# Performance work log

Hardware: AMD Instinct MI355X
Metric: run time of the kernel (lower is better)

The kernel has to match this reference:

```python
import jax, jax.numpy as jnp
import numpy as np

HID = 768
HEADS = 12
HEAD_LEN = HID // HEADS
SCALE_INV = 1.0 / np.sqrt(HEAD_LEN).astype(np.float32)


def setup_inputs() -> dict:
    key = jax.random.key(0)
    ks = jax.random.split(key, 5)
    std = 1.0 / np.sqrt(HID)
    return {
        "x": jax.random.normal(ks[0], (1, 4096, HID), dtype=jnp.float32),
        "w_q": jax.random.normal(ks[1], (HID, HID), dtype=jnp.float32) * std,
        "w_k": jax.random.normal(ks[2], (HID, HID), dtype=jnp.float32) * std,
        "w_v": jax.random.normal(ks[3], (HID, HID), dtype=jnp.float32) * std,
        "w_fc": jax.random.normal(ks[4], (HID, HID), dtype=jnp.float32) * std,
    }


def reference(x, w_q, w_k, w_v, w_fc):
    B, S, D = x.shape
    # torch Linear weight layout [out, in]: y = x @ W.T
    def proj_heads(w):
        y = jnp.einsum("bsd,ed->bse", x, w)
        return y.reshape(B, S, HEADS, HEAD_LEN).transpose(0, 2, 1, 3)  # bhsd
    q = proj_heads(w_q)
    k = proj_heads(w_k)
    v = proj_heads(w_v)
    scores = SCALE_INV * jnp.einsum("bhqd,bhkd->bhqk", q, k)
    attn = jax.nn.softmax(scores, axis=-1)
    out = jnp.einsum("bhqk,bhkd->bhqd", attn, v)
    out = out.transpose(0, 2, 1, 3).reshape(B, S, D)
    return jnp.einsum("bsd,ed->bse", out, w_fc)
```

## Files before the change

kernel.cpp:

```cpp
#include <hip/hip_runtime.h>
#include <hip/hip_bf16.h>

#define S_LEN 4096
#define HID 768
#define NHEAD 12
#define HL 64
#define QB 64
#define ORST 68

typedef __attribute__((ext_vector_type(8))) short short8;
typedef __attribute__((ext_vector_type(4))) short s16x4;
typedef __attribute__((ext_vector_type(4))) float f32x4;
using bf16 = __hip_bfloat16;

__device__ __forceinline__ void gl2lds16(const void* g, void* l) {
  __builtin_amdgcn_global_load_lds((__attribute__((address_space(1))) void*)(g),
                                   (__attribute__((address_space(3))) void*)(l),
                                   16, 0, 0);
}

__device__ __forceinline__ f32x4 mfma_bf16(short8 a, short8 b, f32x4 c) {
  return __builtin_amdgcn_mfma_f32_16x16x32_bf16(a, b, c, 0, 0, 0);
}

__device__ __forceinline__ f32x4 mfma16_bf16(s16x4 a, s16x4 b, f32x4 c) {
#if __has_builtin(__builtin_amdgcn_mfma_f32_16x16x16bf16_1k)
  return __builtin_amdgcn_mfma_f32_16x16x16bf16_1k(a, b, c, 0, 0, 0);
#elif __has_builtin(__builtin_amdgcn_mfma_f32_16x16x16_bf16)
  return __builtin_amdgcn_mfma_f32_16x16x16_bf16(a, b, c, 0, 0, 0);
#else
  f32x4 d;
  asm volatile(
      "s_nop 1\n\t"
      "v_mfma_f32_16x16x16_bf16 %0, %1, %2, %3\n\t"
      "s_nop 7\n\t"
      "s_nop 2"
      : "=&v"(d)
      : "v"(a), "v"(b), "v"(c));
  return d;
#endif
}

__device__ __forceinline__ void storeC(float* C, long idx, float v) { C[idx] = v; }
__device__ __forceinline__ void storeC(bf16* C, long idx, float v) { C[idx] = __float2bfloat16(v); }

__global__ __launch_bounds__(256) void cvt_all(
    const float* __restrict__ x, const float* __restrict__ wq,
    const float* __restrict__ wk, const float* __restrict__ wv,
    const float* __restrict__ wfc, bf16* __restrict__ xb, bf16* __restrict__ wqb,
    bf16* __restrict__ wkb, bf16* __restrict__ wvb, bf16* __restrict__ wfcb) {
  const long NX = (long)S_LEN * HID;
  const long NW = (long)HID * HID;
  long i = ((long)blockIdx.x * 256 + threadIdx.x) * 4;
  const float* src;
  bf16* dst;
  long off;
  if (i < NX) {
    src = x; dst = xb; off = i;
  } else {
    long j = i - NX;
    int wsel = (int)(j / NW);
    off = j - (long)wsel * NW;
    src = wsel == 0 ? wq : wsel == 1 ? wk : wsel == 2 ? wv : wfc;
    dst = wsel == 0 ? wqb : wsel == 1 ? wkb : wsel == 2 ? wvb : wfcb;
  }
  float4 v = *(const float4*)(src + off);
  bf16 h0 = __float2bfloat16(v.x), h1 = __float2bfloat16(v.y);
  bf16 h2 = __float2bfloat16(v.z), h3 = __float2bfloat16(v.w);
  ushort4 o;
  o.x = *(unsigned short*)&h0; o.y = *(unsigned short*)&h1;
  o.z = *(unsigned short*)&h2; o.w = *(unsigned short*)&h3;
  *(ushort4*)(dst + off) = o;
}

template <typename OT>
__global__ __launch_bounds__(256) void gemm_bt(
    const bf16* __restrict__ A, const bf16* __restrict__ B0,
    const bf16* __restrict__ B1, const bf16* __restrict__ B2,
    OT* __restrict__ C0, OT* __restrict__ C1, OT* __restrict__ C2, float qscale) {
  constexpr int K = HID;
  __shared__ __align__(16) bf16 As[128 * 32];
  __shared__ __align__(16) bf16 Bs[128 * 32];
  const int z = blockIdx.z;
  const bf16* B = (z == 0) ? B0 : (z == 1) ? B1 : B2;
  OT* C = (z == 0) ? C0 : (z == 1) ? C1 : C2;
  const float sc = (z == 0) ? qscale : 1.0f;
  const int bm = blockIdx.y, bn = blockIdx.x;
  const int t = threadIdx.x, lane = t & 63, w = t >> 6;
  const int wm = w >> 1, wn = w & 1;
  const int q4 = lane >> 4, c16 = lane & 15;
  const int srow = lane >> 2, scol = (lane & 3) * 8;
  const bf16* Ab = A + (long)bm * 128 * K;
  const bf16* Bb = B + (long)bn * 128 * K;
  f32x4 acc[4][4] = {};
  for (int k0 = 0; k0 < K; k0 += 32) {
#pragma unroll
    for (int r = 0; r < 2; ++r) {
      int rowb = r * 64 + w * 16;
      gl2lds16(Ab + (long)(rowb + srow) * K + k0 + scol, &As[rowb * 32]);
      gl2lds16(Bb + (long)(rowb + srow) * K + k0 + scol, &Bs[rowb * 32]);
    }
    __syncthreads();
    short8 af[4], bfv[4];
#pragma unroll
    for (int i = 0; i < 4; ++i)
      af[i] = *(const short8*)&As[(wm * 64 + i * 16 + c16) * 32 + q4 * 8];
#pragma unroll
    for (int j = 0; j < 4; ++j)
      bfv[j] = *(const short8*)&Bs[(wn * 64 + j * 16 + c16) * 32 + q4 * 8];
#pragma unroll
    for (int i = 0; i < 4; ++i)
#pragma unroll
      for (int j = 0; j < 4; ++j)
        acc[i][j] = mfma_bf16(af[i], bfv[j], acc[i][j]);
    __syncthreads();
  }
  const long crow0 = (long)bm * 128 + wm * 64;
  const int ccol0 = bn * 128 + wn * 64;
#pragma unroll
  for (int i = 0; i < 4; ++i)
#pragma unroll
    for (int j = 0; j < 4; ++j)
#pragma unroll
      for (int r = 0; r < 4; ++r) {
        long row = crow0 + i * 16 + q4 * 4 + r;
        int col = ccol0 + j * 16 + c16;
        storeC(C, row * HID + col, sc * acc[i][j][r]);
      }
}

__global__ __launch_bounds__(256) void gemm_fc(const bf16* __restrict__ A,
                                               const bf16* __restrict__ B,
                                               float* __restrict__ C) {
  __shared__ __align__(16) bf16 As[128 * 32];
  __shared__ __align__(16) bf16 Bs[64 * 32];
  const int bm = blockIdx.y, bn = blockIdx.x;
  const int t = threadIdx.x, lane = t & 63, w = t >> 6;
  const int q4 = lane >> 4, c16 = lane & 15;
  const int srow = lane >> 2, scol = (lane & 3) * 8;
  const bf16* Ab = A + (long)bm * 128 * HID;
  const bf16* Bb = B + (long)bn * 64 * HID;
  f32x4 acc[2][4] = {};
  for (int k0 = 0; k0 < HID; k0 += 32) {
#pragma unroll
    for (int r = 0; r < 2; ++r) {
      int rowb = w * 32 + r * 16;
      gl2lds16(Ab + (long)(rowb + srow) * HID + k0 + scol, &As[rowb * 32]);
    }
    gl2lds16(Bb + (long)(w * 16 + srow) * HID + k0 + scol, &Bs[w * 16 * 32]);
    __syncthreads();
    short8 af[2], bfv[4];
#pragma unroll
    for (int i = 0; i < 2; ++i)
      af[i] = *(const short8*)&As[(w * 32 + i * 16 + c16) * 32 + q4 * 8];
#pragma unroll
    for (int j = 0; j < 4; ++j)
      bfv[j] = *(const short8*)&Bs[(j * 16 + c16) * 32 + q4 * 8];
#pragma unroll
    for (int i = 0; i < 2; ++i)
#pragma unroll
      for (int j = 0; j < 4; ++j)
        acc[i][j] = mfma_bf16(af[i], bfv[j], acc[i][j]);
    __syncthreads();
  }
#pragma unroll
  for (int i = 0; i < 2; ++i)
#pragma unroll
    for (int j = 0; j < 4; ++j)
#pragma unroll
      for (int r = 0; r < 4; ++r) {
        long row = (long)bm * 128 + w * 32 + i * 16 + q4 * 4 + r;
        int col = bn * 64 + j * 16 + c16;
        C[row * HID + col] = acc[i][j][r];
      }
}

__global__ __launch_bounds__(256) void transpose_v(const bf16* __restrict__ V,
                                                   bf16* __restrict__ Vt) {
  __shared__ unsigned short tile[64][65];
  const int bs = blockIdx.x * 64;
  const int be = blockIdx.y * 64;
  const int t = threadIdx.x;
#pragma unroll
  for (int p = 0; p < 4; ++p) {
    int i = p * 256 + t;
    int r = i >> 4;
    int c = (i & 15) * 4;
    ushort4 v = *(const ushort4*)((const unsigned short*)V + (long)(bs + r) * HID + be + c);
    tile[r][c] = v.x; tile[r][c + 1] = v.y; tile[r][c + 2] = v.z; tile[r][c + 3] = v.w;
  }
  __syncthreads();
#pragma unroll
  for (int p = 0; p < 4; ++p) {
    int i = p * 256 + t;
    int r = i >> 4;
    int c = (i & 15) * 4;
    ushort4 v;
    v.x = tile[c][r]; v.y = tile[c + 1][r]; v.z = tile[c + 2][r]; v.w = tile[c + 3][r];
    *(ushort4*)((unsigned short*)Vt + (long)(be + r) * S_LEN + bs + c) = v;
  }
}

__global__ __launch_bounds__(256, 3) void flash_attn(const bf16* __restrict__ Q,
                                                     const bf16* __restrict__ Kg,
                                                     const bf16* __restrict__ Vt,
                                                     bf16* __restrict__ O) {
  __shared__ float Ored[64 * ORST];
  __shared__ float Lred[4][QB];
  const int i0 = blockIdx.x;
  const int xcd = i0 & 7, sb = i0 >> 3;
  const int pair = xcd >> 1;
  const int r2 = sb * 2 + (xcd & 1);
  const int h = pair * 3 + (r2 >> 6);
  const int qt = r2 & 63;
  const int t = threadIdx.x, lane = t & 63, w = t >> 6;
  const int q4 = lane >> 4, c16 = lane & 15;
  const int s0 = qt * QB;

  short8 qf[2][4];
  {
    const bf16* Qb = Q + (long)(s0 + c16) * HID + h * HL + q4 * 8;
#pragma unroll
    for (int j = 0; j < 4; ++j)
#pragma unroll
      for (int ks = 0; ks < 2; ++ks)
        qf[ks][j] = *(const short8*)(Qb + (long)j * 16 * HID + ks * 32);
  }
  const bf16* kp = Kg + (long)(w * 16 + c16) * HID + h * HL + q4 * 8;
  const bf16* vbase = Vt + (long)(h * HL + c16) * S_LEN + w * 16 + q4 * 4;

  float l_part[4] = {0.f, 0.f, 0.f, 0.f};
  f32x4 o_acc[4][4] = {};

  short8 kf0 = *(const short8*)(kp), kf1 = *(const short8*)(kp + 32);

  constexpr int NT = S_LEN / 64;
  for (int kt = 0; kt < NT; ++kt) {
    const bf16* kpn = (kt + 1 < NT) ? kp + 64 * HID : kp;
    short8 nk0 = *(const short8*)(kpn), nk1 = *(const short8*)(kpn + 32);
    s16x4 vf[4];
#pragma unroll
    for (int i = 0; i < 4; ++i)
      vf[i] = *(const s16x4*)(vbase + (long)i * 16 * S_LEN + kt * 64);

    f32x4 sacc[4] = {};
#pragma unroll
    for (int j = 0; j < 4; ++j) sacc[j] = mfma_bf16(kf0, qf[0][j], sacc[j]);
#pragma unroll
    for (int j = 0; j < 4; ++j) sacc[j] = mfma_bf16(kf1, qf[1][j], sacc[j]);

#pragma unroll
    for (int j = 0; j < 4; ++j) {
      float p0 = __builtin_amdgcn_exp2f(sacc[j][0]);
      float p1 = __builtin_amdgcn_exp2f(sacc[j][1]);
      float p2 = __builtin_amdgcn_exp2f(sacc[j][2]);
      float p3 = __builtin_amdgcn_exp2f(sacc[j][3]);
      l_part[j] += (p0 + p1) + (p2 + p3);
      bf16 b0 = __float2bfloat16(p0), b1 = __float2bfloat16(p1);
      bf16 b2 = __float2bfloat16(p2), b3 = __float2bfloat16(p3);
      s16x4 pf;
      pf[0] = *(short*)&b0; pf[1] = *(short*)&b1;
      pf[2] = *(short*)&b2; pf[3] = *(short*)&b3;
#pragma unroll
      for (int i = 0; i < 4; ++i)
        o_acc[i][j] = mfma16_bf16(vf[i], pf, o_acc[i][j]);
    }

    kf0 = nk0; kf1 = nk1; kp = kpn;
  }

#pragma unroll
  for (int j = 0; j < 4; ++j) {
    float s = l_part[j];
    s += __shfl_xor(s, 16, 64);
    s += __shfl_xor(s, 32, 64);
    Lred[w][j * 16 + c16] = s;
  }
  __syncthreads();
  float rl[4];
#pragma unroll
  for (int j = 0; j < 4; ++j) {
    int q = j * 16 + c16;
    rl[j] = 1.0f / (Lred[0][q] + Lred[1][q] + Lred[2][q] + Lred[3][q]);
  }

#pragma unroll
  for (int rd = 0; rd < 4; ++rd) {
#pragma unroll
    for (int j = 0; j < 4; ++j)
#pragma unroll
      for (int r = 0; r < 4; ++r)
        Ored[(w * 16 + q4 * 4 + r) * ORST + j * 16 + c16] = o_acc[rd][j][r];
    __syncthreads();
    if (w == rd) {
#pragma unroll
      for (int j = 0; j < 4; ++j) {
        float v[4];
#pragma unroll
        for (int r = 0; r < 4; ++r) {
          int off = (q4 * 4 + r) * ORST + j * 16 + c16;
          v[r] = (Ored[off] + Ored[16 * ORST + off]) +
                 (Ored[32 * ORST + off] + Ored[48 * ORST + off]);
          v[r] *= rl[j];
        }
        bf16 b0 = __float2bfloat16(v[0]), b1 = __float2bfloat16(v[1]);
        bf16 b2 = __float2bfloat16(v[2]), b3 = __float2bfloat16(v[3]);
        short4 pk;
        pk.x = *(short*)&b0; pk.y = *(short*)&b1;
        pk.z = *(short*)&b2; pk.w = *(short*)&b3;
        *(short4*)&O[(long)(s0 + j * 16 + c16) * HID + h * HL + rd * 16 + q4 * 4] = pk;
      }
    }
    __syncthreads();
  }
}

extern "C" void kernel_launch(void* const* d_in, const int* in_sizes, int n_in,
                              void* d_out, int out_size, void* d_ws, size_t ws_size,
                              hipStream_t stream) {
  const float* x = (const float*)d_in[0];
  const float* wq = (const float*)d_in[1];
  const float* wk = (const float*)d_in[2];
  const float* wv = (const float*)d_in[3];
  const float* wfc = (const float*)d_in[4];
  float* out = (float*)d_out;

  const long NBIG = (long)S_LEN * HID * sizeof(bf16);
  const long NWB = (long)HID * HID * sizeof(bf16);
  char* p = (char*)d_ws;
  bf16* xb = (bf16*)p;   p += NBIG;
  bf16* wqb = (bf16*)p;  p += NWB;
  bf16* wkb = (bf16*)p;  p += NWB;
  bf16* wvb = (bf16*)p;  p += NWB;
  bf16* wfcb = (bf16*)p; p += NWB;
  bf16* Qb = (bf16*)p;   p += NBIG;
  bf16* Kb = (bf16*)p;   p += NBIG;
  bf16* Vb = (bf16*)p;   p += NBIG;
  bf16* Vtb = (bf16*)p;  p += NBIG;
  bf16* Ob = (bf16*)p;   p += NBIG;

  const float c1 = 0.125f * 1.44269504088896340736f;

  const long total4 = ((long)S_LEN * HID + 4L * HID * HID) / 4;
  cvt_all<<<(int)(total4 / 256), 256, 0, stream>>>(x, wq, wk, wv, wfc, xb, wqb, wkb,
                                                   wvb, wfcb);
  gemm_bt<bf16><<<dim3(HID / 128, S_LEN / 128, 3), 256, 0, stream>>>(
      xb, wqb, wkb, wvb, Qb, Kb, Vb, c1);
  transpose_v<<<dim3(S_LEN / 64, HID / 64), 256, 0, stream>>>(Vb, Vtb);
  flash_attn<<<dim3(S_LEN / QB * NHEAD), 256, 0, stream>>>(Qb, Kb, Vtb, Ob);
  gemm_fc<<<dim3(HID / 64, S_LEN / 128), 256, 0, stream>>>(Ob, wfcb, out);
}
```

Before: 254.5 us.

## Software-pipeline flash attention loop: overlap QK MFMA with previous tile's PV

Result: no change. 254.0 us (-0.2%).

```diff
diff --git a/kernel.cpp b/kernel.cpp
--- a/kernel.cpp
+++ b/kernel.cpp
@@ -216,6 +216,7 @@
   const int t = threadIdx.x, lane = t & 63, w = t >> 6;
   const int q4 = lane >> 4, c16 = lane & 15;
   const int s0 = qt * QB;
+  constexpr int NT = S_LEN / 64;
 
   short8 qf[2][4];
   {
@@ -231,24 +232,18 @@
 
   float l_part[4] = {0.f, 0.f, 0.f, 0.f};
   f32x4 o_acc[4][4] = {};
-
-  short8 kf0 = *(const short8*)(kp), kf1 = *(const short8*)(kp + 32);
-
-  constexpr int NT = S_LEN / 64;
-  for (int kt = 0; kt < NT; ++kt) {
-    const bf16* kpn = (kt + 1 < NT) ? kp + 64 * HID : kp;
-    short8 nk0 = *(const short8*)(kpn), nk1 = *(const short8*)(kpn + 32);
-    s16x4 vf[4];
-#pragma unroll
-    for (int i = 0; i < 4; ++i)
-      vf[i] = *(const s16x4*)(vbase + (long)i * 16 * S_LEN + kt * 64);
-
+  s16x4 pfA[4], pfB[4];
+  s16x4 vf[4];
+  short8 kf0, kf1;
+
+  kf0 = *(const short8*)kp;
+  kf1 = *(const short8*)(kp + 32);
+  {
     f32x4 sacc[4] = {};
 #pragma unroll
     for (int j = 0; j < 4; ++j) sacc[j] = mfma_bf16(kf0, qf[0][j], sacc[j]);
 #pragma unroll
     for (int j = 0; j < 4; ++j) sacc[j] = mfma_bf16(kf1, qf[1][j], sacc[j]);
-
 #pragma unroll
     for (int j = 0; j < 4; ++j) {
       float p0 = __builtin_amdgcn_exp2f(sacc[j][0]);
@@ -258,16 +253,59 @@
       l_part[j] += (p0 + p1) + (p2 + p3);
       bf16 b0 = __float2bfloat16(p0), b1 = __float2bfloat16(p1);
       bf16 b2 = __float2bfloat16(p2), b3 = __float2bfloat16(p3);
-      s16x4 pf;
-      pf[0] = *(short*)&b0; pf[1] = *(short*)&b1;
-      pf[2] = *(short*)&b2; pf[3] = *(short*)&b3;
-#pragma unroll
-      for (int i = 0; i < 4; ++i)
-        o_acc[i][j] = mfma16_bf16(vf[i], pf, o_acc[i][j]);
+      pfA[j][0] = *(short*)&b0; pfA[j][1] = *(short*)&b1;
+      pfA[j][2] = *(short*)&b2; pfA[j][3] = *(short*)&b3;
     }
-
-    kf0 = nk0; kf1 = nk1; kp = kpn;
-  }
+  }
+  kp += 64 * HID;
+  kf0 = *(const short8*)kp;
+  kf1 = *(const short8*)(kp + 32);
+#pragma unroll
+  for (int i = 0; i < 4; ++i)
+    vf[i] = *(const s16x4*)(vbase + (long)i * 16 * S_LEN);
+
+#define FA_BODY(T, PFU, PFM)                                                   \
+  {                                                                            \
+    f32x4 sacc[4] = {};                                                        \
+    _Pragma("unroll") for (int j = 0; j < 4; ++j)                              \
+        sacc[j] = mfma_bf16(kf0, qf[0][j], sacc[j]);                           \
+    _Pragma("unroll") for (int j = 0; j < 4; ++j)                              \
+        sacc[j] = mfma_bf16(kf1, qf[1][j], sacc[j]);                           \
+    const bf16* kpn_ = ((T) + 2 < NT) ? kp + 64 * HID : kp;                    \
+    kf0 = *(const short8*)(kpn_);                                              \
+    kf1 = *(const short8*)(kpn_ + 32);                                         \
+    kp = kpn_;                                                                 \
+    _Pragma("unroll") for (int j = 0; j < 4; ++j)                              \
+        _Pragma("unroll") for (int i = 0; i < 4; ++i)                          \
+            o_acc[i][j] = mfma16_bf16(vf[i], PFU[j], o_acc[i][j]);             \
+    const bf16* vpn_ = vbase + (long)(((T) + 1 < NT) ? (T) + 1 : (T)) * 64;    \
+    _Pragma("unroll") for (int i = 0; i < 4; ++i)                              \
+        vf[i] = *(const s16x4*)(vpn_ + (long)i * 16 * S_LEN);                  \
+    _Pragma("unroll") for (int j = 0; j < 4; ++j) {                            \
+      float p0 = __builtin_amdgcn_exp2f(sacc[j][0]);                           \
+      float p1 = __builtin_amdgcn_exp2f(sacc[j][1]);                           \
+      float p2 = __builtin_amdgcn_exp2f(sacc[j][2]);                           \
+      float p3 = __builtin_amdgcn_exp2f(sacc[j][3]);                           \
+      l_part[j] += (p0 + p1) + (p2 + p3);                                      \
+      bf16 b0 = __float2bfloat16(p0), b1 = __float2bfloat16(p1);               \
+      bf16 b2 = __float2bfloat16(p2), b3 = __float2bfloat16(p3);               \
+      PFM[j][0] = *(short*)&b0; PFM[j][1] = *(short*)&b1;                      \
+      PFM[j][2] = *(short*)&b2; PFM[j][3] = *(short*)&b3;                      \
+    }                                                                          \
+  }
+
+  for (int T = 0; T < 62; T += 2) {
+    FA_BODY(T, pfA, pfB);
+    FA_BODY(T + 1, pfB, pfA);
+  }
+  FA_BODY(62, pfA, pfB);
+#undef FA_BODY
+
+#pragma unroll
+  for (int j = 0; j < 4; ++j)
+#pragma unroll
+    for (int i = 0; i < 4; ++i)
+      o_acc[i][j] = mfma16_bf16(vf[i], pfB[j], o_acc[i][j]);
 
 #pragma unroll
   for (int j = 0; j < 4; ++j) {
```
